# Optimization experiments

Measured on AMD Instinct MI355X. Metric: run time of the kernel, lower is better.

Reference implementation:

```python
import jax, jax.numpy as jnp
import numpy as np

DIM, H, C = 1024, 16, 64
D = DIM // H  # head_dim = 64
GATE_HID = 16


def setup_inputs() -> dict:
    key = jax.random.key(0)
    ks = jax.random.split(key, 8)
    B, L = 2, 2048

    def xav(k, fan_in, fan_out):
        return jax.random.normal(k, (fan_in, fan_out), jnp.float32) * np.sqrt(2.0 / (fan_in + fan_out))

    return {
        "x": jax.random.normal(ks[0], (B, L, DIM), jnp.float32),
        "Wq": xav(ks[1], DIM, DIM), "bq": jnp.zeros((DIM,), jnp.float32),
        "Wk": xav(ks[2], DIM, DIM), "bk": jnp.zeros((DIM,), jnp.float32),
        "Wv": xav(ks[3], DIM, DIM), "bv": jnp.zeros((DIM,), jnp.float32),
        "Wg1": xav(ks[4], DIM, GATE_HID), "bg1": jnp.zeros((GATE_HID,), jnp.float32),
        "Wg2": xav(ks[5], GATE_HID, H * D), "bg2": jnp.zeros((H * D,), jnp.float32),
    }


def reference(x, Wq, bq, Wk, bk, Wv, bv, Wg1, bg1, Wg2, bg2):
    B, L, dim = x.shape
    pad = (-L) % C
    if pad:
        x = jnp.pad(x, ((0, 0), (0, pad), (0, 0)))
    Lp = L + pad

    def proj(W, b):
        # (B, Lp, dim) -> (B, H, Lp, D)
        return (x @ W + b).reshape(B, Lp, H, D).transpose(0, 2, 1, 3)

    q, k, v = proj(Wq, bq), proj(Wk, bk), proj(Wv, bv)
    gate = jax.nn.sigmoid(jax.nn.silu(x @ Wg1 + bg1) @ Wg2 + bg2)
    alpha = 0.9 * gate.reshape(B, Lp, H, D).transpose(0, 2, 1, 3) + 0.1  # (B,H,Lp,D)

    # --- intra-chunk causal softmax attention (vectorized over chunks) ---
    Nc = Lp // C
    qc = q.reshape(B, H, Nc, C, D)
    kc = k.reshape(B, H, Nc, C, D)
    vc = v.reshape(B, H, Nc, C, D)
    scores = jnp.einsum('bhncd,bhnkd->bhnck', qc, kc) / np.sqrt(D).astype(np.float32)
    causal = jnp.tril(jnp.ones((C, C), bool))
    scores = jnp.where(causal, scores, -jnp.inf)
    intra = jnp.einsum('bhnck,bhnke->bhnce', jax.nn.softmax(scores, axis=-1), vc)
    intra = intra.reshape(B, H, Lp, D)

    # --- inter: gated linear-attention recurrence over the full sequence ---
    # Note: in the original code S is updated every timestep (including inside
    # chunks), so the 'inter' term at step t sees ALL tokens < t, not just
    # previous chunks.
    def step(S, inp):
        q_t, k_t, v_t, a_t = inp  # each (B, H, D)
        inter_t = jnp.einsum('bhd,bhde->bhe', q_t, S)
        S = a_t[..., None] * S + k_t[..., None] * v_t[..., None, :]
        return S, inter_t

    xs = tuple(a.transpose(2, 0, 1, 3) for a in (q, k, v, alpha))  # (Lp, B, H, D)
    S0 = jnp.zeros((B, H, D, D), x.dtype)
    _, inter = jax.lax.scan(step, S0, xs)  # (Lp, B, H, D)
    inter = inter.transpose(1, 2, 0, 3)  # (B, H, Lp, D)

    out = (inter + intra).transpose(0, 2, 1, 3).reshape(B, Lp, dim)
    return out[:, :L]
```

## Files before the change

kernel.cpp:

```cpp
#include <hip/hip_runtime.h>
#include <math.h>

#define DIMN 1024
#define NH 16
#define HD 64
#define CHK 64
#define NB 2
#define SEQ 2048
#define NTOK (NB*SEQ)
#define NCHUNK (SEQ/CHK)
#define GH 16

typedef __bf16 bf16x8 __attribute__((ext_vector_type(8)));
typedef float f32x4 __attribute__((ext_vector_type(4)));
typedef unsigned short u16x4 __attribute__((ext_vector_type(4)));

__device__ __forceinline__ unsigned short f2bf(float f) {
  union { float f; unsigned u; } a; a.f = f;
  unsigned r = a.u + 0x7FFFu + ((a.u >> 16) & 1u);
  return (unsigned short)(r >> 16);
}
__device__ __forceinline__ float bf2f(unsigned short v) {
  union { unsigned u; float f; } a; a.u = ((unsigned)v) << 16;
  return a.f;
}

__device__ __forceinline__ void gload16(const void* g, void* l) {
  __builtin_amdgcn_global_load_lds(
      (const __attribute__((address_space(1))) void*)g,
      (__attribute__((address_space(3))) void*)l, 16, 0, 0);
}

__global__ __launch_bounds__(256) void k_cast_wT(const float* __restrict__ W0,
    const float* __restrict__ W1, const float* __restrict__ W2,
    unsigned short* __restrict__ wt) {
  __shared__ float tile[64][68];
  int z = blockIdx.z;
  const float* W = z==0 ? W0 : z==1 ? W1 : W2;
  unsigned short* o = wt + (size_t)z*DIMN*DIMN;
  int k0 = blockIdx.y*64, n0 = blockIdx.x*64;
  int tr = threadIdx.x >> 4, c0 = (threadIdx.x & 15)*4;
  #pragma unroll
  for (int s = 0; s < 4; ++s) {
    int r = tr + s*16;
    *(f32x4*)&tile[r][c0] = *(const f32x4*)(W + (size_t)(k0+r)*DIMN + n0 + c0);
  }
  __syncthreads();
  #pragma unroll
  for (int s = 0; s < 4; ++s) {
    int nn = tr + s*16;
    ushort4 v;
    v.x = f2bf(tile[c0+0][nn]);
    v.y = f2bf(tile[c0+1][nn]);
    v.z = f2bf(tile[c0+2][nn]);
    v.w = f2bf(tile[c0+3][nn]);
    *(ushort4*)(o + (size_t)(n0+nn)*DIMN + k0 + c0) = v;
  }
}

__global__ __launch_bounds__(256) void k_wg1t(const float* __restrict__ Wg1,
    unsigned short* __restrict__ wg1b) {
  int idx = blockIdx.x*256 + threadIdx.x;
  int k = idx & 1023, j = idx >> 10;
  wg1b[j*DIMN + k] = f2bf(Wg1[k*GH + j]);
}

__global__ __launch_bounds__(256) void k_castx_hidden(const float* __restrict__ x,
    const unsigned short* __restrict__ wg1b, const float* __restrict__ bg1,
    unsigned short* __restrict__ xb, float* __restrict__ hid) {
  __shared__ __align__(16) unsigned short xs[16][1032];
  __shared__ float red[4][16][16];
  int tid = threadIdx.x;
  size_t base = (size_t)blockIdx.x * 16 * DIMN;
  #pragma unroll
  for (int i = 0; i < 16; ++i) {
    int idx4 = tid + i*256;
    int r = idx4 >> 8, c4 = idx4 & 255;
    f32x4 v = *(const f32x4*)(x + base + (size_t)idx4*4);
    u16x4 o;
    o[0]=f2bf(v[0]); o[1]=f2bf(v[1]); o[2]=f2bf(v[2]); o[3]=f2bf(v[3]);
    *(u16x4*)&xs[r][c4*4] = o;
    *(u16x4*)(xb + base + (size_t)idx4*4) = o;
  }
  __syncthreads();
  int l = tid & 63, w = tid >> 6;
  int lr = l & 15, kg = l >> 4;
  union FB { uint4 u; bf16x8 h; } a, b;
  f32x4 acc = {0.f,0.f,0.f,0.f};
  const unsigned short* wrow = wg1b + (size_t)lr*DIMN + w*256 + kg*8;
  #pragma unroll
  for (int kk = 0; kk < 8; ++kk) {
    a.u = *(const uint4*)&xs[lr][w*256 + kk*32 + kg*8];
    b.u = *(const uint4*)(wrow + kk*32);
    acc = __builtin_amdgcn_mfma_f32_16x16x32_bf16(a.h, b.h, acc, 0, 0, 0);
  }
  #pragma unroll
  for (int rg = 0; rg < 4; ++rg) red[w][kg*4 + rg][lr] = acc[rg];
  __syncthreads();
  {
    int m = tid >> 4, j = tid & 15;
    float s = red[0][m][j] + red[1][m][j] + red[2][m][j] + red[3][m][j];
    s += bg1[j];
    hid[(blockIdx.x*16 + m)*GH + j] = s / (1.f + expf(-s));
  }
}

__global__ __launch_bounds__(256, 3) void k_projqkv(const unsigned short* __restrict__ xb,
    const unsigned short* __restrict__ wt,
    const float* __restrict__ b0, const float* __restrict__ b1, const float* __restrict__ b2,
    unsigned short* __restrict__ o0, unsigned short* __restrict__ o1,
    unsigned short* __restrict__ o2) {
  __shared__ unsigned short As[3][128*32];
  __shared__ unsigned short Bs[3][128*32];
  int tid = threadIdx.x;
  int wg = blockIdx.y * gridDim.x + blockIdx.x;
  int swz = (wg & 7) * 96 + (wg >> 3);
  int bx = swz % 24, by = swz / 24;
  int n3 = bx*128;
  int z = n3 >> 10;
  int n0l = n3 & 1023;
  const float* bias = z==0 ? b0 : z==1 ? b1 : b2;
  unsigned short* out = z==0 ? o0 : z==1 ? o1 : o2;
  int m0 = by*128;

  int l = tid & 63;
  int w = tid >> 6;
  int wr = w >> 1, wc = w & 1;
  int lrow = l & 15, kg = l >> 4;

  f32x4 acc[4][4] = {};

  int r0s = tid >> 2, s0s = tid & 3;
  int r1s = (tid + 256) >> 2;
  int sg0 = s0s ^ ((r0s >> 1) & 3);
  int sg1 = s0s ^ ((r1s >> 1) & 3);

  #define STAGE(buf, kt) do { \
    int kb_ = (kt)*32; \
    gload16(xb + ((size_t)(m0 + r0s)*DIMN + kb_ + sg0*8), &As[buf][tid*8]); \
    gload16(wt + ((size_t)(n3 + r0s)*DIMN + kb_ + sg0*8), &Bs[buf][tid*8]); \
    gload16(xb + ((size_t)(m0 + r1s)*DIMN + kb_ + sg1*8), &As[buf][(tid+256)*8]); \
    gload16(wt + ((size_t)(n3 + r1s)*DIMN + kb_ + sg1*8), &Bs[buf][(tid+256)*8]); \
  } while (0)

  STAGE(0, 0);
  STAGE(1, 1);
  for (int t = 0; t < DIMN/32; ++t) {
    if (t < DIMN/32 - 1) {
      asm volatile("s_waitcnt vmcnt(4)" ::: "memory");
    } else {
      asm volatile("s_waitcnt vmcnt(0)" ::: "memory");
    }
    __builtin_amdgcn_s_barrier();
    if (t+2 < DIMN/32) STAGE((t+2)%3, t+2);
    int buf = t % 3;
    union { uint4 u; bf16x8 h; } af[4], bfr[4];
    #pragma unroll
    for (int mf = 0; mf < 4; ++mf) {
      int r = wr*64 + mf*16 + lrow;
      int slot = kg ^ ((r >> 1) & 3);
      af[mf].u = *(const uint4*)&As[buf][r*32 + slot*8];
    }
    #pragma unroll
    for (int nf = 0; nf < 4; ++nf) {
      int r = wc*64 + nf*16 + lrow;
      int slot = kg ^ ((r >> 1) & 3);
      bfr[nf].u = *(const uint4*)&Bs[buf][r*32 + slot*8];
    }
    #pragma unroll
    for (int mf = 0; mf < 4; ++mf)
      #pragma unroll
      for (int nf = 0; nf < 4; ++nf)
        acc[mf][nf] = __builtin_amdgcn_mfma_f32_16x16x32_bf16(
            af[mf].h, bfr[nf].h, acc[mf][nf], 0, 0, 0);
  }
  #undef STAGE

  float bv[4];
  #pragma unroll
  for (int nf = 0; nf < 4; ++nf) bv[nf] = bias[n0l + wc*64 + nf*16 + lrow];
  #pragma unroll
  for (int mf = 0; mf < 4; ++mf) {
    int rbase = m0 + wr*64 + mf*16 + kg*4;
    #pragma unroll
    for (int nf = 0; nf < 4; ++nf) {
      int c = n0l + wc*64 + nf*16 + lrow;
      #pragma unroll
      for (int rg = 0; rg < 4; ++rg)
        out[(size_t)(rbase+rg)*DIMN + c] = f2bf(acc[mf][nf][rg] + bv[nf]);
    }
  }
}

__global__ __launch_bounds__(256, 4) void k_ginc(const unsigned short* __restrict__ kbuf,
    const unsigned short* __restrict__ vbuf,
    const float* __restrict__ hid, const float* __restrict__ Wg2,
    const float* __restrict__ bg2,
    unsigned short* __restrict__ G, float* __restrict__ Bv) {
  __shared__ __align__(16) unsigned short kb16[64*72];
  __shared__ __align__(16) unsigned short vT[64*72];
  __shared__ __align__(16) unsigned short kdT[64*72];
  __shared__ __align__(16) float scr[2048];
  __shared__ float seg[4][64];
  int tid = threadIdx.x;
  int bid = blockIdx.x;
  int bh = bid >> 5, n = bid & 31;
  int b = bh >> 4, h = bh & 15;
  int colbase = h*HD;
  size_t rowbase = (size_t)b*SEQ + n*CHK;

  {
    int r = tid >> 2, j0 = (tid & 3)*4;
    *(f32x4*)&scr[r*16 + j0] = *(const f32x4*)(hid + (rowbase + r)*GH + j0);
    int j = tid >> 4, d0 = (tid & 15)*4;
    *(f32x4*)&scr[1024 + j*64 + d0] = *(const f32x4*)(Wg2 + (size_t)j*DIMN + colbase + d0);
  }
  #pragma unroll
  for (int i = 0; i < 4; ++i) {
    int f4 = tid + i*256;
    int r = f4 >> 4, cg = f4 & 15, c0 = cg*4;
    size_t g = (rowbase + r)*DIMN + colbase + c0;
    u16x4 k4 = *(const u16x4*)(kbuf + g);
    u16x4 v4 = *(const u16x4*)(vbuf + g);
    *(u16x4*)&kb16[r*72 + c0] = k4;
    #pragma unroll
    for (int j = 0; j < 4; ++j) vT[(c0+j)*72 + r] = v4[j];
  }
  __syncthreads();

  {
    int d = tid & 63, ig = tid >> 6;
    float wcol[16];
    #pragma unroll
    for (int j = 0; j < 16; ++j) wcol[j] = scr[1024 + j*64 + d];
    float bgd = bg2[colbase + d];
    float P[16];
    float run = 0.f;
    #pragma unroll
    for (int t = 0; t < 16; ++t) {
      int i = ig*16 + t;
      float acc = bgd;
      #pragma unroll
      for (int j = 0; j < 16; ++j) acc = fmaf(scr[i*16 + j], wcol[j], acc);
      float gg = 1.f/(1.f + expf(-acc));
      run += log2f(fmaf(0.9f, gg, 0.1f));
      P[t] = run;
    }
    seg[ig][d] = run;
    __syncthreads();
    float s0 = seg[0][d], s1 = seg[1][d], s2 = seg[2][d], s3 = seg[3][d];
    float carry = (ig > 0 ? s0 : 0.f) + (ig > 1 ? s1 : 0.f) + (ig > 2 ? s2 : 0.f);
    float Lb63 = s0 + s1 + s2 + s3;
    if (ig == 0) Bv[(size_t)bid*HD + d] = exp2f(Lb63);
    union { unsigned short s[16]; uint4 u[2]; } kd;
    #pragma unroll
    for (int t = 0; t < 16; ++t) {
      int i = ig*16 + t;
      float kv = bf2f(kb16[i*72 + d]);
      kd.s[t] = f2bf(kv * exp2f(Lb63 - carry - P[t]));
    }
    *(uint4*)&kdT[d*72 + ig*16] = kd.u[0];
    *(uint4*)&kdT[d*72 + ig*16 + 8] = kd.u[1];
  }
  __syncthreads();

  int l = tid & 63, w = tid >> 6;
  int lr = l & 15, kg = l >> 4;
  int ks = kg*8;
  int arow = w*16 + lr;
  union FB { uint4 u; bf16x8 h; } a0, a1;
  a0.u = *(const uint4*)&kdT[arow*72 + ks];
  a1.u = *(const uint4*)&kdT[arow*72 + 32 + ks];
  unsigned short* gp = G + (size_t)bid*(HD*HD);
  #pragma unroll
  for (int nf = 0; nf < 4; ++nf) {
    FB b0v, b1v;
    b0v.u = *(const uint4*)&vT[(nf*16+lr)*72 + ks];
    b1v.u = *(const uint4*)&vT[(nf*16+lr)*72 + 32 + ks];
    f32x4 z = {0.f,0.f,0.f,0.f};
    z = __builtin_amdgcn_mfma_f32_16x16x32_bf16(a0.h, b0v.h, z, 0,0,0);
    z = __builtin_amdgcn_mfma_f32_16x16x32_bf16(a1.h, b1v.h, z, 0,0,0);
    #pragma unroll
    for (int rg = 0; rg < 4; ++rg)
      gp[(w*16 + kg*4 + rg)*HD + nf*16 + lr] = f2bf(z[rg]);
  }
}

__global__ __launch_bounds__(256) void k_scan(unsigned short* __restrict__ buf,
    const float* __restrict__ Bv) {
  int idx = blockIdx.x*256 + threadIdx.x;
  int e = idx & 63, d = (idx >> 6) & 63, bh = idx >> 12;
  unsigned short* gp = buf + (size_t)bh*NCHUNK*HD*HD + d*HD + e;
  const float* bp = Bv + (size_t)bh*NCHUNK*HD + d;
  float g[NCHUNK], bb[NCHUNK];
  #pragma unroll
  for (int n = 0; n < NCHUNK; ++n) g[n] = bf2f(gp[n*(HD*HD)]);
  #pragma unroll
  for (int n = 0; n < NCHUNK; ++n) bb[n] = bp[n*HD];
  float s = 0.f;
  #pragma unroll
  for (int n = 0; n < NCHUNK; ++n) {
    gp[n*(HD*HD)] = f2bf(s);
    s = fmaf(bb[n], s, g[n]);
  }
}

__global__ __launch_bounds__(256) void k_chunk(const unsigned short* __restrict__ qbuf,
    const unsigned short* __restrict__ kbuf, const unsigned short* __restrict__ vbuf,
    const float* __restrict__ hid, const float* __restrict__ Wg2,
    const float* __restrict__ bg2,
    const unsigned short* __restrict__ states, float* __restrict__ outp) {
  __shared__ __align__(16) unsigned short qb16[64*72];
  __shared__ __align__(16) unsigned short kb16[64*72];
  __shared__ __align__(16) unsigned short vT[64*72];
  __shared__ __align__(16) unsigned short Pl[64*72];
  __shared__ __align__(16) unsigned short Swt[2][64*72];
  __shared__ __align__(16) float lb[65*68];
  __shared__ __align__(16) unsigned short dgs[4][16*40];
  __shared__ float seg[4][64];

  const int tid = threadIdx.x;
  const int bid = blockIdx.x;
  const int bh = bid >> 5, n = bid & 31;
  const int b = bh >> 4, h = bh & 15;
  const int colbase = h*HD;
  const size_t rowbase = (size_t)b*SEQ + n*CHK;
  const unsigned short* stp = states + (size_t)(bh*NCHUNK + n)*(HD*HD);

  float* scr = (float*)Pl;
  {
    int r = tid >> 2, j0 = (tid & 3)*4;
    *(f32x4*)&scr[r*16 + j0] = *(const f32x4*)(hid + (rowbase + r)*GH + j0);
  }
  #pragma unroll
  for (int i = 0; i < 4; ++i) {
    int f4 = tid + i*256;
    int r = f4 >> 4, cg = f4 & 15, c0 = cg*4;
    size_t g = (rowbase + r)*DIMN + colbase + c0;
    u16x4 q4 = *(const u16x4*)(qbuf + g);
    u16x4 k4 = *(const u16x4*)(kbuf + g);
    u16x4 v4 = *(const u16x4*)(vbuf + g);
    u16x4 s4 = *(const u16x4*)(stp + r*HD + c0);
    #pragma unroll
    for (int j = 0; j < 4; ++j) {
      vT[(c0+j)*72 + r] = v4[j];
      Swt[0][(c0+j)*72 + r] = s4[j];
    }
    *(u16x4*)&qb16[r*72 + c0] = q4;
    *(u16x4*)&kb16[r*72 + c0] = k4;
  }
  __syncthreads();

  {
    int d = tid & 63, ig = tid >> 6;
    float wcol[16];
    #pragma unroll
    for (int j = 0; j < 16; ++j) wcol[j] = Wg2[(size_t)j*DIMN + colbase + d];
    float bgd = bg2[colbase + d];
    float Pex[16];
    float run = 0.f;
    #pragma unroll
    for (int t = 0; t < 16; ++t) {
      int i = ig*16 + t;
      float acc = bgd;
      #pragma unroll
      for (int j = 0; j < 16; ++j) acc = fmaf(scr[i*16 + j], wcol[j], acc);
      float gg = 1.f/(1.f + expf(-acc));
      Pex[t] = run;
      run += log2f(fmaf(0.9f, gg, 0.1f));
    }
    seg[ig][d] = run;
    __syncthreads();
    float carry = 0.f;
    for (int w2 = 0; w2 < ig; ++w2) carry += seg[w2][d];
    #pragma unroll
    for (int t = 0; t < 16; ++t)
      lb[(ig*16 + t)*68 + d] = carry + Pex[t];
    if (ig == 3) lb[64*68 + d] = carry + run;
  }
  __syncthreads();

  const int l = tid & 63, w = tid >> 6;
  const int lr = l & 15, lg = l >> 4;
  const int ks = lg*8;
  const int arow = w*16 + lr;

  union FB { uint4 u; bf16x8 h; unsigned short s[8]; };

  FB qa0, qa1;
  qa0.u = *(const uint4*)&qb16[arow*72 + ks];
  qa1.u = *(const uint4*)&qb16[arow*72 + 32 + ks];
  f32x4 sc[4];
  __builtin_amdgcn_s_setprio(1);
  #pragma unroll
  for (int nf = 0; nf < 4; ++nf) {
    FB b0, b1;
    b0.u = *(const uint4*)&kb16[(nf*16+lr)*72 + ks];
    b1.u = *(const uint4*)&kb16[(nf*16+lr)*72 + 32 + ks];
    f32x4 z = {0.f,0.f,0.f,0.f};
    z = __builtin_amdgcn_mfma_f32_16x16x32_bf16(qa0.h, b0.h, z, 0,0,0);
    z = __builtin_amdgcn_mfma_f32_16x16x32_bf16(qa1.h, b1.h, z, 0,0,0);
    sc[nf] = z;
  }
  __builtin_amdgcn_s_setprio(0);

  float rmax[4] = {-3e38f,-3e38f,-3e38f,-3e38f};
  #pragma unroll
  for (int nf = 0; nf < 4; ++nf) {
    int col = nf*16 + lr;
    #pragma unroll
    for (int rg = 0; rg < 4; ++rg) {
      int row = w*16 + lg*4 + rg;
      float v = sc[nf][rg]*0.125f;
      if (col > row) v = -1e30f;
      sc[nf][rg] = v;
      rmax[rg] = fmaxf(rmax[rg], v);
    }
  }
  #pragma unroll
  for (int m = 1; m <= 8; m <<= 1)
    #pragma unroll
    for (int rg = 0; rg < 4; ++rg)
      rmax[rg] = fmaxf(rmax[rg], __shfl_xor(rmax[rg], m));
  float rsum[4] = {0.f,0.f,0.f,0.f};
  #pragma unroll
  for (int nf = 0; nf < 4; ++nf)
    #pragma unroll
    for (int rg = 0; rg < 4; ++rg) {
      float e = exp2f((sc[nf][rg] - rmax[rg])*1.44269504f);
      sc[nf][rg] = e;
      rsum[rg] += e;
    }
  #pragma unroll
  for (int m = 1; m <= 8; m <<= 1)
    #pragma unroll
    for (int rg = 0; rg < 4; ++rg)
      rsum[rg] += __shfl_xor(rsum[rg], m);
  #pragma unroll
  for (int nf = 0; nf < 4; ++nf)
    #pragma unroll
    for (int rg = 0; rg < 4; ++rg)
      Pl[(w*16 + lg*4 + rg)*72 + nf*16 + lr] = f2bf(sc[nf][rg]);
  float inv[4];
  #pragma unroll
  for (int rg = 0; rg < 4; ++rg) inv[rg] = 1.f/rsum[rg];
  __syncthreads();

  f32x4 acc[4];
  {
    FB p0, p1;
    p0.u = *(const uint4*)&Pl[arow*72 + ks];
    p1.u = *(const uint4*)&Pl[arow*72 + 32 + ks];
    __builtin_amdgcn_s_setprio(1);
    #pragma unroll
    for (int nf = 0; nf < 4; ++nf) {
      FB v0, v1;
      v0.u = *(const uint4*)&vT[(nf*16+lr)*72 + ks];
      v1.u = *(const uint4*)&vT[(nf*16+lr)*72 + 32 + ks];
      f32x4 z = {0.f,0.f,0.f,0.f};
      z = __builtin_amdgcn_mfma_f32_16x16x32_bf16(p0.h, v0.h, z, 0,0,0);
      z = __builtin_amdgcn_mfma_f32_16x16x32_bf16(p1.h, v1.h, z, 0,0,0);
      #pragma unroll
      for (int rg = 0; rg < 4; ++rg)
        acc[nf][rg] = z[rg]*inv[rg];
    }
    __builtin_amdgcn_s_setprio(0);
  }

  {
    int dA = arow;
    float lb32 = lb[32*68 + dA];
    FB ku;
    #pragma unroll
    for (int j = 0; j < 8; ++j) {
      int s = ks + j;
      float kv = bf2f(kb16[s*72 + dA]);
      ku.s[j] = f2bf(kv * exp2f(lb32 - lb[(s+1)*68 + dA]));
    }
    int d0 = w*16 + lg*4;
    float bs[4];
    #pragma unroll
    for (int rg = 0; rg < 4; ++rg) bs[rg] = exp2f(lb[32*68 + d0 + rg]);
    __builtin_amdgcn_s_setprio(1);
    #pragma unroll
    for (int nf = 0; nf < 4; ++nf) {
      int e = nf*16 + lr;
      FB vv;
      vv.u = *(const uint4*)&vT[e*72 + ks];
      f32x4 z = {0.f,0.f,0.f,0.f};
      z = __builtin_amdgcn_mfma_f32_16x16x32_bf16(ku.h, vv.h, z, 0,0,0);
      u16x4 s0v = *(const u16x4*)&Swt[0][e*72 + d0];
      u16x4 s1v;
      #pragma unroll
      for (int rg = 0; rg < 4; ++rg)
        s1v[rg] = f2bf(z[rg] + bs[rg]*bf2f(s0v[rg]));
      *(u16x4*)&Swt[1][e*72 + d0] = s1v;
    }
    __builtin_amdgcn_s_setprio(0);
  }
  __syncthreads();

  {
    const int T = (w >= 2) ? 32 : 0;
    const unsigned short* Ssel = (w >= 2) ? &Swt[1][0] : &Swt[0][0];
    FB qd[2];
    #pragma unroll
    for (int kst = 0; kst < 2; ++kst) {
      int ds = kst*32 + ks;
      f32x4 lbi0 = *(const f32x4*)&lb[arow*68 + ds];
      f32x4 lbi1 = *(const f32x4*)&lb[arow*68 + ds + 4];
      f32x4 lbt0 = *(const f32x4*)&lb[T*68 + ds];
      f32x4 lbt1 = *(const f32x4*)&lb[T*68 + ds + 4];
      FB qr;
      qr.u = *(const uint4*)&qb16[arow*72 + ds];
      #pragma unroll
      for (int j = 0; j < 4; ++j) {
        qd[kst].s[j]   = f2bf(bf2f(qr.s[j])   * exp2f(lbi0[j] - lbt0[j]));
        qd[kst].s[4+j] = f2bf(bf2f(qr.s[4+j]) * exp2f(lbi1[j] - lbt1[j]));
      }
    }
    __builtin_amdgcn_s_setprio(1);
    #pragma unroll
    for (int nf = 0; nf < 4; ++nf) {
      FB s0f, s1f;
      s0f.u = *(const uint4*)&Ssel[(nf*16+lr)*72 + ks];
      s1f.u = *(const uint4*)&Ssel[(nf*16+lr)*72 + 32 + ks];
      acc[nf] = __builtin_amdgcn_mfma_f32_16x16x32_bf16(qd[0].h, s0f.h, acc[nf], 0,0,0);
      acc[nf] = __builtin_amdgcn_mfma_f32_16x16x32_bf16(qd[1].h, s1f.h, acc[nf], 0,0,0);
    }
    __builtin_amdgcn_s_setprio(0);
    const int nb_ = (w & 1) ? 2 : 1;
    f32x4 dgc[2] = {{0.f,0.f,0.f,0.f},{0.f,0.f,0.f,0.f}};
    #pragma unroll
    for (int bf_ = 0; bf_ < 2; ++bf_) {
      if (bf_ < nb_) {
        int s = T + bf_*16 + lr;
        f32x4 z = {0.f,0.f,0.f,0.f};
        #pragma unroll
        for (int kst = 0; kst < 2; ++kst) {
          int ds = kst*32 + ks;
          f32x4 lbt0 = *(const f32x4*)&lb[T*68 + ds];
          f32x4 lbt1 = *(const f32x4*)&lb[T*68 + ds + 4];
          f32x4 lbs0 = *(const f32x4*)&lb[(s+1)*68 + ds];
          f32x4 lbs1 = *(const f32x4*)&lb[(s+1)*68 + ds + 4];
          FB kr, kd;
          kr.u = *(const uint4*)&kb16[s*72 + ds];
          #pragma unroll
          for (int j = 0; j < 4; ++j) {
            kd.s[j]   = f2bf(bf2f(kr.s[j])   * exp2f(lbt0[j] - lbs0[j]));
            kd.s[4+j] = f2bf(bf2f(kr.s[4+j]) * exp2f(lbt1[j] - lbs1[j]));
          }
          z = __builtin_amdgcn_mfma_f32_16x16x32_bf16(qd[kst].h, kd.h, z, 0,0,0);
        }
        dgc[bf_] = z;
      }
    }
    int iis = (w & 1)*16 + lg*4;
    #pragma unroll
    for (int bf_ = 0; bf_ < 2; ++bf_) {
      #pragma unroll
      for (int rg = 0; rg < 4; ++rg) {
        int ssu = bf_*16 + lr;
        float v = (bf_ < nb_ && ssu < iis + rg) ? dgc[bf_][rg] : 0.f;
        dgs[w][(lg*4 + rg)*40 + bf_*16 + lr] = f2bf(v);
      }
    }
    FB dga;
    dga.u = *(const uint4*)&dgs[w][lr*40 + ks];
    __builtin_amdgcn_s_setprio(1);
    #pragma unroll
    for (int nf = 0; nf < 4; ++nf) {
      FB vv;
      vv.u = *(const uint4*)&vT[(nf*16+lr)*72 + T + ks];
      acc[nf] = __builtin_amdgcn_mfma_f32_16x16x32_bf16(dga.h, vv.h, acc[nf], 0,0,0);
    }
    __builtin_amdgcn_s_setprio(0);
  }

  #pragma unroll
  for (int nf = 0; nf < 4; ++nf)
    #pragma unroll
    for (int rg = 0; rg < 4; ++rg)
      outp[(rowbase + w*16 + lg*4 + rg)*DIMN + colbase + nf*16 + lr] = acc[nf][rg];
}

extern "C" void kernel_launch(void* const* d_in, const int* in_sizes, int n_in,
                              void* d_out, int out_size, void* d_ws, size_t ws_size,
                              hipStream_t stream) {
  const float* x   = (const float*)d_in[0];
  const float* Wq  = (const float*)d_in[1];
  const float* bq  = (const float*)d_in[2];
  const float* Wk  = (const float*)d_in[3];
  const float* bk  = (const float*)d_in[4];
  const float* Wv  = (const float*)d_in[5];
  const float* bv  = (const float*)d_in[6];
  const float* Wg1 = (const float*)d_in[7];
  const float* bg1 = (const float*)d_in[8];
  const float* Wg2 = (const float*)d_in[9];
  const float* bg2 = (const float*)d_in[10];
  float* out = (float*)d_out;

  float* ws = (float*)d_ws;
  const size_t NT = (size_t)NTOK*DIMN;
  const size_t NST = (size_t)NB*NH*NCHUNK*HD*HD;
  float* hid = ws;
  float* Bv  = hid + (size_t)NTOK*GH;
  unsigned short* stb = (unsigned short*)(Bv + (size_t)NB*NH*NCHUNK*HD);
  unsigned short* xb = stb + NST;
  unsigned short* wt = xb + NT;
  unsigned short* wg1b = wt + 3*(size_t)DIMN*DIMN;
  unsigned short* qb = wg1b + (size_t)GH*DIMN;
  unsigned short* kb = qb + NT;
  unsigned short* vb = kb + NT;

  k_cast_wT<<<dim3(16, 16, 3), 256, 0, stream>>>(Wq, Wk, Wv, wt);
  k_wg1t<<<(GH*DIMN)/256, 256, 0, stream>>>(Wg1, wg1b);
  k_castx_hidden<<<NTOK/16, 256, 0, stream>>>(x, wg1b, bg1, xb, hid);
  k_projqkv<<<dim3(24, 32), 256, 0, stream>>>(
      xb, wt, bq, bk, bv, qb, kb, vb);
  k_ginc<<<NB*NH*NCHUNK, 256, 0, stream>>>(kb, vb, hid, Wg2, bg2, stb, Bv);
  k_scan<<<(NB*NH*HD*HD)/256, 256, 0, stream>>>(stb, Bv);
  k_chunk<<<NB*NH*NCHUNK, 256, 0, stream>>>(qb, kb, vb, hid, Wg2, bg2, stb, out);
}
```

Before: 93.32 us.

## Enlarge QKV projection GEMM tiles to 256x256x64 with 512 threads, double buffered

Rewrites the fused QKV projection GEMM to use 256x256 output tiles with a K-step of 64, 512 threads (8 waves each computing 128x64), and two LDS buffers instead of three. Larger tiles raise arithmetic intensity and cut global reloads of x and W. The grid drops from 768 to 192 workgroups, which is below one wave of blocks on a 256-CU device. The change also uses more LDS and accumulator registers per wave, adds a second barrier per iteration, and keeps the XOR swizzle adapted to 8 slots.

```diff
diff --git a/kernel.cpp b/kernel.cpp
--- a/kernel.cpp
+++ b/kernel.cpp
@@ -105,86 +105,87 @@
   }
 }
 
-__global__ __launch_bounds__(256, 3) void k_projqkv(const unsigned short* __restrict__ xb,
+__global__ __launch_bounds__(512, 2) void k_projqkv(const unsigned short* __restrict__ xb,
     const unsigned short* __restrict__ wt,
     const float* __restrict__ b0, const float* __restrict__ b1, const float* __restrict__ b2,
     unsigned short* __restrict__ o0, unsigned short* __restrict__ o1,
     unsigned short* __restrict__ o2) {
-  __shared__ unsigned short As[3][128*32];
-  __shared__ unsigned short Bs[3][128*32];
+  __shared__ unsigned short As[2][256*64];
+  __shared__ unsigned short Bs[2][256*64];
   int tid = threadIdx.x;
-  int wg = blockIdx.y * gridDim.x + blockIdx.x;
-  int swz = (wg & 7) * 96 + (wg >> 3);
-  int bx = swz % 24, by = swz / 24;
-  int n3 = bx*128;
-  int z = n3 >> 10;
-  int n0l = n3 & 1023;
+  int wg = blockIdx.x;
+  int swz = (wg & 7) * 24 + (wg >> 3);
+  int bx = swz % 12, by = swz / 12;
+  int n3 = bx*256;
+  int z = bx >> 2;
+  int n0l = (bx & 3)*256;
   const float* bias = z==0 ? b0 : z==1 ? b1 : b2;
   unsigned short* out = z==0 ? o0 : z==1 ? o1 : o2;
-  int m0 = by*128;
+  int m0 = by*256;
 
   int l = tid & 63;
   int w = tid >> 6;
-  int wr = w >> 1, wc = w & 1;
-  int lrow = l & 15, kg = l >> 4;
-
-  f32x4 acc[4][4] = {};
-
-  int r0s = tid >> 2, s0s = tid & 3;
-  int r1s = (tid + 256) >> 2;
-  int sg0 = s0s ^ ((r0s >> 1) & 3);
-  int sg1 = s0s ^ ((r1s >> 1) & 3);
+  int wr = w >> 2, wc = w & 3;
+  int lr = l & 15, kg = l >> 4;
+
+  f32x4 acc[8][4] = {};
 
   #define STAGE(buf, kt) do { \
-    int kb_ = (kt)*32; \
-    gload16(xb + ((size_t)(m0 + r0s)*DIMN + kb_ + sg0*8), &As[buf][tid*8]); \
-    gload16(wt + ((size_t)(n3 + r0s)*DIMN + kb_ + sg0*8), &Bs[buf][tid*8]); \
-    gload16(xb + ((size_t)(m0 + r1s)*DIMN + kb_ + sg1*8), &As[buf][(tid+256)*8]); \
-    gload16(wt + ((size_t)(n3 + r1s)*DIMN + kb_ + sg1*8), &Bs[buf][(tid+256)*8]); \
+    _Pragma("unroll") \
+    for (int i_ = 0; i_ < 4; ++i_) { \
+      int flat_ = tid + i_*512; \
+      int r_ = flat_ >> 3, s_ = flat_ & 7; \
+      int sg_ = s_ ^ (r_ & 7); \
+      gload16(xb + ((size_t)(m0 + r_)*DIMN + (kt)*64 + sg_*8), &As[buf][flat_*8]); \
+      gload16(wt + ((size_t)(n3 + r_)*DIMN + (kt)*64 + sg_*8), &Bs[buf][flat_*8]); \
+    } \
   } while (0)
 
   STAGE(0, 0);
-  STAGE(1, 1);
-  for (int t = 0; t < DIMN/32; ++t) {
-    if (t < DIMN/32 - 1) {
-      asm volatile("s_waitcnt vmcnt(4)" ::: "memory");
+  for (int t = 0; t < 16; ++t) {
+    if (t+1 < 16) {
+      STAGE((t+1)&1, t+1);
+      asm volatile("s_waitcnt vmcnt(8)" ::: "memory");
     } else {
       asm volatile("s_waitcnt vmcnt(0)" ::: "memory");
     }
     __builtin_amdgcn_s_barrier();
-    if (t+2 < DIMN/32) STAGE((t+2)%3, t+2);
-    int buf = t % 3;
-    union { uint4 u; bf16x8 h; } af[4], bfr[4];
-    #pragma unroll
-    for (int mf = 0; mf < 4; ++mf) {
-      int r = wr*64 + mf*16 + lrow;
-      int slot = kg ^ ((r >> 1) & 3);
-      af[mf].u = *(const uint4*)&As[buf][r*32 + slot*8];
-    }
+    const unsigned short* Ab = &As[t&1][0];
+    const unsigned short* Bb = &Bs[t&1][0];
+    #pragma unroll
+    for (int kst = 0; kst < 2; ++kst) {
+      union FBv { uint4 u; bf16x8 h; } bfr[4];
+      #pragma unroll
+      for (int nf = 0; nf < 4; ++nf) {
+        int R = wc*64 + nf*16 + lr;
+        int s_ = (kst*4 + kg) ^ (R & 7);
+        bfr[nf].u = *(const uint4*)&Bb[R*64 + s_*8];
+      }
+      #pragma unroll
+      for (int mf = 0; mf < 8; ++mf) {
+        int R = wr*128 + mf*16 + lr;
+        int s_ = (kst*4 + kg) ^ (R & 7);
+        union FBv { uint4 u; bf16x8 h; } af;
+        af.u = *(const uint4*)&Ab[R*64 + s_*8];
+        #pragma unroll
+        for (int nf = 0; nf < 4; ++nf)
+          acc[mf][nf] = __builtin_amdgcn_mfma_f32_16x16x32_bf16(
+              af.h, bfr[nf].h, acc[mf][nf], 0, 0, 0);
+      }
+    }
+    __builtin_amdgcn_s_barrier();
+  }
+  #undef STAGE
+
+  float bv[4];
+  #pragma unroll
+  for (int nf = 0; nf < 4; ++nf) bv[nf] = bias[n0l + wc*64 + nf*16 + lr];
+  #pragma unroll
+  for (int mf = 0; mf < 8; ++mf) {
+    int rbase = m0 + wr*128 + mf*16 + kg*4;
     #pragma unroll
     for (int nf = 0; nf < 4; ++nf) {
-      int r = wc*64 + nf*16 + lrow;
-      int slot = kg ^ ((r >> 1) & 3);
-      bfr[nf].u = *(const uint4*)&Bs[buf][r*32 + slot*8];
-    }
-    #pragma unroll
-    for (int mf = 0; mf < 4; ++mf)
-      #pragma unroll
-      for (int nf = 0; nf < 4; ++nf)
-        acc[mf][nf] = __builtin_amdgcn_mfma_f32_16x16x32_bf16(
-            af[mf].h, bfr[nf].h, acc[mf][nf], 0, 0, 0);
-  }
-  #undef STAGE
-
-  float bv[4];
-  #pragma unroll
-  for (int nf = 0; nf < 4; ++nf) bv[nf] = bias[n0l + wc*64 + nf*16 + lrow];
-  #pragma unroll
-  for (int mf = 0; mf < 4; ++mf) {
-    int rbase = m0 + wr*64 + mf*16 + kg*4;
-    #pragma unroll
-    for (int nf = 0; nf < 4; ++nf) {
-      int c = n0l + wc*64 + nf*16 + lrow;
+      int c = n0l + wc*64 + nf*16 + lr;
       #pragma unroll
       for (int rg = 0; rg < 4; ++rg)
         out[(size_t)(rbase+rg)*DIMN + c] = f2bf(acc[mf][nf][rg] + bv[nf]);
@@ -616,7 +617,7 @@
   k_cast_wT<<<dim3(16, 16, 3), 256, 0, stream>>>(Wq, Wk, Wv, wt);
   k_wg1t<<<(GH*DIMN)/256, 256, 0, stream>>>(Wg1, wg1b);
   k_castx_hidden<<<NTOK/16, 256, 0, stream>>>(x, wg1b, bg1, xb, hid);
-  k_projqkv<<<dim3(24, 32), 256, 0, stream>>>(
+  k_projqkv<<<192, 512, 0, stream>>>(
       xb, wt, bq, bk, bv, qb, kb, vb);
   k_ginc<<<NB*NH*NCHUNK, 256, 0, stream>>>(kb, vb, hid, Wg2, bg2, stb, Bv);
   k_scan<<<(NB*NH*HD*HD)/256, 256, 0, stream>>>(stb, Bv);
```

Result: slower. 96.54 us (+3.5%).
